# Optimization experiments

Measured on AMD Instinct MI355X. Metric: run time of the kernel, lower is better.

## Reference

```python
import jax, jax.numpy as jnp
import numpy as np

N_QUBITS = 8
N_LAYERS = 3
N_CLASSES = 3
BATCH = 16384


def setup_inputs() -> dict:
    key = jax.random.key(0)
    k1, k2, k3, k4 = jax.random.split(key, 4)
    x = jax.random.uniform(k1, (BATCH, N_QUBITS), dtype=jnp.float32)  # PCA feats in [0,1]
    q_weights = jax.random.normal(k2, (N_LAYERS * 2 * N_QUBITS,), dtype=jnp.float32) * 0.1
    W = jax.random.normal(k3, (N_CLASSES, N_CLASSES), dtype=jnp.float32) / np.sqrt(N_CLASSES)
    b = jax.random.normal(k4, (N_CLASSES,), dtype=jnp.float32) * 0.1
    return {"x": x, "q_weights": q_weights, "W": W, "b": b}


def _ry(state, wire, theta):
    """Batched RY(theta) on `wire`. state: (B,)+(2,)*n, theta: (B,)."""
    ax = 1 + wire
    s0 = jnp.take(state, 0, axis=ax)
    s1 = jnp.take(state, 1, axis=ax)
    bshape = (theta.shape[0],) + (1,) * (s0.ndim - 1)
    c = jnp.cos(0.5 * theta).reshape(bshape)
    s = jnp.sin(0.5 * theta).reshape(bshape)
    return jnp.stack([c * s0 - s * s1, s * s0 + c * s1], axis=ax)


def _rz(state, wire, theta):
    """RZ(theta) on `wire`, theta scalar: diag(e^{-i t/2}, e^{i t/2})."""
    ax = 1 + wire
    phases = jnp.stack([jnp.exp(-0.5j * theta), jnp.exp(0.5j * theta)])
    shape = (1,) * ax + (2,) + (1,) * (state.ndim - ax - 1)
    return state * phases.reshape(shape)


def _cnot(state, ctrl, tgt):
    """CNOT: flip target bit on the control=1 slice."""
    cax = 1 + ctrl
    a0 = jnp.take(state, 0, axis=cax)
    a1 = jnp.take(state, 1, axis=cax)
    # control axis was removed; target axis shifts down by one if tgt > ctrl
    tax = 1 + tgt if tgt < ctrl else tgt
    a1 = jnp.flip(a1, axis=tax)
    return jnp.stack([a0, a1], axis=cax)


def _circuit(x, q_weights):
    B = x.shape[0]
    state = jnp.zeros((B, 2 ** N_QUBITS), dtype=jnp.complex64).at[:, 0].set(1.0)
    state = state.reshape((B,) + (2,) * N_QUBITS)
    for layer in range(N_LAYERS):
        base = layer * 2 * N_QUBITS
        for i in range(N_QUBITS):
            state = _ry(state, i, x[:, i] * np.pi + q_weights[base + i])
        for i in range(N_QUBITS - 1):
            state = _cnot(state, i, i + 1)
        state = _cnot(state, N_QUBITS - 1, 0)
        for i in range(N_QUBITS):
            state = _rz(state, i, q_weights[base + N_QUBITS + i])
    probs = state.real ** 2 + state.imag ** 2  # (B,)+(2,)*n
    zs = []
    for i in range(N_CLASSES):
        ax = 1 + i
        p = probs.sum(axis=tuple(a for a in range(1, N_QUBITS + 1) if a != ax))  # (B,2)
        zs.append(p[:, 0] - p[:, 1])  # <Z_i>
    return jnp.stack(zs, axis=1).astype(jnp.float32)  # (B, n_classes)


def reference(x, q_weights, W, b):
    q_out = _circuit(x, q_weights)
    return q_out @ W.T + b
```

## Files before the change

### kernel.cpp

```cpp
#include <hip/hip_runtime.h>
#include <math.h>

#define NQ 8
#define NL 3
#define NC 3
#define BATCH 16384


__device__ __forceinline__ int par(int x) { return __popc(x) & 1; }

template<int CTRL>
__device__ __forceinline__ float dppmov(float v) {
  return __builtin_bit_cast(float,
    __builtin_amdgcn_update_dpp(0, __builtin_bit_cast(int, v), CTRL, 0xF, 0xF, true));
}

template<int M>
__device__ __forceinline__ float xl(float v) {
  static_assert(M > 0 && M < 64, "mask range");
  if constexpr (M < 16) {
    constexpr int hi = M & 12;
    constexpr int first = (hi == 0) ? 0 : (hi == 4) ? 0x141
                          : (hi == 8) ? 0x128
                          : 0x140;
    constexpr int qx = (hi == 4 || hi == 12) ? ((M & 3) ^ 3) : (M & 3);
    constexpr int qc = (qx == 1) ? 0xB1 : (qx == 2) ? 0x4E : 0x1B;
    float t = v;
    if constexpr (first != 0) t = dppmov<first>(t);
    if constexpr (qx != 0)    t = dppmov<qc>(t);
    return t;
  } else if constexpr (M < 32) {
    return __builtin_bit_cast(float,
      __builtin_amdgcn_ds_swizzle(__builtin_bit_cast(int, v), (M << 10) | 0x1F));
  } else {
    const int li = (int)(threadIdx.x & 63);
    return __builtin_bit_cast(float,
      __builtin_amdgcn_ds_bpermute(((li ^ M) << 2), __builtin_bit_cast(int, v)));
  }
}


template<int UREG, int GREG, int GLANE>
__device__ __forceinline__ void ry_rr(float (&sr)[4], float (&si)[4],
                                      float c, float s, int q) {
  static_assert((__builtin_popcount(UREG & GREG) & 1) == 1, "<g,u>!=1");
  const float sl = par(q & GLANE) ? s : -s;
  #pragma unroll
  for (int rA = 0; rA < 4; ++rA) {
    if (rA < (rA ^ UREG)) {
      const int rB = rA ^ UREG;
      const float FA = (__builtin_popcount(rA & GREG) & 1) ? -sl : sl;
      const float ar = sr[rA], ai = si[rA];
      sr[rA] = c * ar + FA * sr[rB];
      si[rA] = c * ai + FA * si[rB];
      sr[rB] = c * sr[rB] - FA * ar;
      si[rB] = c * si[rB] - FA * ai;
    }
  }
}

template<int ULANE, int GREG, int GLANE>
__device__ __forceinline__ void ry_ll(float (&sr)[4], float (&si)[4],
                                      float c, float s, int q) {
  static_assert((__builtin_popcount(ULANE & GLANE) & 1) == 1, "<g,u>!=1");
  const float sl = par(q & GLANE) ? s : -s;
  #pragma unroll
  for (int r = 0; r < 4; ++r) {
    const float xr = xl<ULANE>(sr[r]);
    const float xi = xl<ULANE>(si[r]);
    const float F  = (__builtin_popcount(r & GREG) & 1) ? -sl : sl;
    sr[r] = c * sr[r] + F * xr;
    si[r] = c * si[r] + F * xi;
  }
}

template<int UREG, int ULANE, int GREG, int GLANE>
__device__ __forceinline__ void ry_mix(float (&sr)[4], float (&si)[4],
                                       float c, float s, int q) {
  static_assert(((__builtin_popcount(UREG & GREG) + __builtin_popcount(ULANE & GLANE)) & 1) == 1,
                "<g,u>!=1");
  constexpr int RFLIP = __builtin_popcount(GREG & UREG) & 1;
  const float sl = par(q & GLANE) ? s : -s;
  #pragma unroll
  for (int rA = 0; rA < 4; ++rA) {
    if (rA < (rA ^ UREG)) {
      const int rB = rA ^ UREG;
      const float pBr = xl<ULANE>(sr[rB]);
      const float pBi = xl<ULANE>(si[rB]);
      const float pAr = xl<ULANE>(sr[rA]);
      const float pAi = xl<ULANE>(si[rA]);
      const float FA = (__builtin_popcount(rA & GREG) & 1) ? -sl : sl;
      const float FB = RFLIP ? -FA : FA;
      sr[rA] = c * sr[rA] + FA * pBr;
      si[rA] = c * si[rA] + FA * pBi;
      sr[rB] = c * sr[rB] + FB * pAr;
      si[rB] = c * si[rB] + FB * pAi;
    }
  }
}

__global__ __launch_bounds__(256, 6) void vqc_kernel(
    const float* __restrict__ x, const float* __restrict__ qw,
    const float* __restrict__ W, const float* __restrict__ b,
    float* __restrict__ out)
{
  const int tid  = threadIdx.x;
  const int q    = tid & 63;
  const int elem = blockIdx.x * 4 + (tid >> 6);

  const float PI = 3.14159265358979323846f;

  float xs[8];
  {
    const float4 x0 = *(const float4*)(x + elem * 8);
    const float4 x1 = *(const float4*)(x + elem * 8 + 4);
    xs[0] = x0.x; xs[1] = x0.y; xs[2] = x0.z; xs[3] = x0.w;
    xs[4] = x1.x; xs[5] = x1.y; xs[6] = x1.z; xs[7] = x1.w;
  }

  float sr[4], si[4];

  {
    float c0_, s0_, c1_, s1_;
    __sincosf(0.5f * (PI * xs[0] + qw[0]), &s0_, &c0_);
    __sincosf(0.5f * (PI * xs[1] + qw[1]), &s1_, &c1_);
    float P = 1.f;
    #pragma unroll
    for (int w = 2; w < 8; ++w) {
      float s_, c_;
      __sincosf(0.5f * (PI * xs[w] + qw[w]), &s_, &c_);
      P *= ((q >> (w - 2)) & 1) ? s_ : c_;
    }
    sr[0] = P * c0_ * c1_;
    sr[1] = P * s0_ * c1_;
    sr[2] = P * c0_ * s1_;
    sr[3] = P * s0_ * s1_;
  }

  {
    const float h0 = 0.5f * qw[8],  h1 = 0.5f * qw[9];
    const float h2 = 0.5f * qw[10], h3 = 0.5f * qw[11];
    const float h4 = 0.5f * qw[12], h5 = 0.5f * qw[13];
    const float h6 = 0.5f * qw[14], h7 = 0.5f * qw[15];
    const float a0 = par(q & 63) ? h0 : -h0;
    const float B  = -h1 + (par(q & 1)  ? h2 : -h2) + (par(q & 3)  ? h3 : -h3)
                         + (par(q & 7)  ? h4 : -h4) + (par(q & 15) ? h5 : -h5)
                         + (par(q & 31) ? h6 : -h6) + (par(q & 63) ? h7 : -h7);
    float sp0, cp0, sp1, cp1;
    __sincosf(a0 + B, &sp0, &cp0);
    __sincosf(a0 - B, &sp1, &cp1);
    si[0] =  sp0 * sr[0]; sr[0] *= cp0;
    si[1] =  sp1 * sr[1]; sr[1] *= cp1;
    si[2] = -sp0 * sr[2]; sr[2] *= cp0;
    si[3] = -sp1 * sr[3]; sr[3] *= cp1;
  }

  {
    float c_, s_;
    __sincosf(0.5f * (PI * xs[0] + qw[16]), &s_, &c_); ry_rr <3,     2, 63>(sr, si, c_, s_, q);
    __sincosf(0.5f * (PI * xs[1] + qw[17]), &s_, &c_); ry_mix<2, 1,  3,  0>(sr, si, c_, s_, q);
    __sincosf(0.5f * (PI * xs[2] + qw[18]), &s_, &c_); ry_ll <3,     3,  1>(sr, si, c_, s_, q);
    __sincosf(0.5f * (PI * xs[3] + qw[19]), &s_, &c_); ry_ll <6,     3,  3>(sr, si, c_, s_, q);
    __sincosf(0.5f * (PI * xs[4] + qw[20]), &s_, &c_); ry_ll <12,    3,  7>(sr, si, c_, s_, q);
    __sincosf(0.5f * (PI * xs[5] + qw[21]), &s_, &c_); ry_ll <24,    3, 15>(sr, si, c_, s_, q);
    __sincosf(0.5f * (PI * xs[6] + qw[22]), &s_, &c_); ry_ll <48,    3, 31>(sr, si, c_, s_, q);
    __sincosf(0.5f * (PI * xs[7] + qw[23]), &s_, &c_); ry_mix<3, 32, 3, 63>(sr, si, c_, s_, q);
  }

  {
    const float h0 = 0.5f * qw[24], h1 = 0.5f * qw[25];
    const float h2 = 0.5f * qw[26], h3 = 0.5f * qw[27];
    const float h4 = 0.5f * qw[28], h5 = 0.5f * qw[29];
    const float h6 = 0.5f * qw[30], h7 = 0.5f * qw[31];
    const float t0 = par(q & 42) ? h0 : -h0;
    const float D1 = (par(q & 63) ? h1 : -h1) + (par(q & 61) ? h3 : -h3)
                   + (par(q & 53) ? h5 : -h5) + (par(q & 21) ? h7 : -h7);
    const float D2 = (par(q & 62) ? h2 : -h2) + (par(q & 58) ? h4 : -h4)
                   + (par(q & 42) ? h6 : -h6);
    const float ph[4] = { t0 + D1 + D2, -t0 - D1 + D2,
                          -t0 + D1 - D2,  t0 - D1 - D2 };
    #pragma unroll
    for (int r = 0; r < 4; ++r) {
      float sp, cp;
      __sincosf(ph[r], &sp, &cp);
      const float re = sr[r], im = si[r];
      sr[r] = cp * re - sp * im;
      si[r] = cp * im + sp * re;
    }
  }

  {
    float c_, s_;
    __sincosf(0.5f * (PI * xs[0] + qw[32]), &s_, &c_); ry_mix<1, 1,  3, 42>(sr, si, c_, s_, q);
    __sincosf(0.5f * (PI * xs[1] + qw[33]), &s_, &c_); ry_mix<2, 2,  1, 63>(sr, si, c_, s_, q);
    __sincosf(0.5f * (PI * xs[2] + qw[34]), &s_, &c_); ry_ll <5,     2, 62>(sr, si, c_, s_, q);
    __sincosf(0.5f * (PI * xs[3] + qw[35]), &s_, &c_); ry_ll <10,    1, 61>(sr, si, c_, s_, q);
    __sincosf(0.5f * (PI * xs[4] + qw[36]), &s_, &c_); ry_ll <20,    2, 58>(sr, si, c_, s_, q);
    __sincosf(0.5f * (PI * xs[5] + qw[37]), &s_, &c_); ry_ll <40,    1, 53>(sr, si, c_, s_, q);
    __sincosf(0.5f * (PI * xs[6] + qw[38]), &s_, &c_); ry_mix<3, 16, 2, 42>(sr, si, c_, s_, q);
    __sincosf(0.5f * (PI * xs[7] + qw[39]), &s_, &c_); ry_mix<2, 33, 1, 21>(sr, si, c_, s_, q);
  }

  const float p0 = sr[0] * sr[0] + si[0] * si[0];
  const float p1 = sr[1] * sr[1] + si[1] * si[1];
  const float p2 = sr[2] * sr[2] + si[2] * si[2];
  const float p3 = sr[3] * sr[3] + si[3] * si[3];
  const float ta = (p0 + p1) - (p2 + p3);
  const float tb =  p0 + p1 + p2 + p3;
  float z0 = par(q & 12) ? -ta : ta;
  float z1 = par(q & 21) ? -ta : ta;
  float z2 = par(q & 43) ? -tb : tb;

  z0 += xl<1>(z0);  z1 += xl<1>(z1);  z2 += xl<1>(z2);
  z0 += xl<2>(z0);  z1 += xl<2>(z1);  z2 += xl<2>(z2);
  z0 += xl<4>(z0);  z1 += xl<4>(z1);  z2 += xl<4>(z2);
  z0 += xl<8>(z0);  z1 += xl<8>(z1);  z2 += xl<8>(z2);
  z0 += xl<16>(z0); z1 += xl<16>(z1); z2 += xl<16>(z2);
  z0 += xl<32>(z0); z1 += xl<32>(z1); z2 += xl<32>(z2);

  if (q < NC) {
    out[elem * NC + q] = b[q] + W[q * 3 + 0] * z0 + W[q * 3 + 1] * z1
                              + W[q * 3 + 2] * z2;
  }
}

extern "C" void kernel_launch(void* const* d_in, const int* in_sizes, int n_in,
                              void* d_out, int out_size, void* d_ws, size_t ws_size,
                              hipStream_t stream) {
  const float* x  = (const float*)d_in[0];
  const float* qw = (const float*)d_in[1];
  const float* W  = (const float*)d_in[2];
  const float* b  = (const float*)d_in[3];
  float* out = (float*)d_out;

  dim3 grid(BATCH / 4);
  vqc_kernel<<<grid, 256, 0, stream>>>(x, qw, W, b, out);
}
```

Measured before the change: 26.48 us.

## Use permlane swaps for cross-row exchanges, batch sincos, raise occupancy bound

Replaces ds_swizzle/ds_bpermute lane exchanges for masks 16 and 32 with permlane16/32 swap builtins when available. Exchanges whose mask mixes high and low bits become a chain of permlane and DPP moves. The per-gate sincos calls are hoisted into batched arrays ahead of each RY layer so transcendental latency can overlap, and launch bounds move from 6 to 8 waves. The aim is to avoid LDS-path shuffle latency and raise ILP and occupancy, at the cost of more live registers and possible spills under the tighter bound.

```diff
diff --git a/kernel.cpp b/kernel.cpp
--- a/kernel.cpp
+++ b/kernel.cpp
@@ -15,28 +15,51 @@
     __builtin_amdgcn_update_dpp(0, __builtin_bit_cast(int, v), CTRL, 0xF, 0xF, true));
 }
 
+__device__ __forceinline__ float pl16(float v) {
+#if __has_builtin(__builtin_amdgcn_permlane16_swap)
+  typedef int i2 __attribute__((ext_vector_type(2)));
+  const int iv = __builtin_bit_cast(int, v);
+  i2 pr = __builtin_amdgcn_permlane16_swap(iv, iv, false, false);
+  const int lane = (int)(threadIdx.x & 63);
+  return __builtin_bit_cast(float, (lane & 16) ? pr[0] : pr[1]);
+#else
+  return __builtin_bit_cast(float,
+    __builtin_amdgcn_ds_swizzle(__builtin_bit_cast(int, v), (16 << 10) | 0x1F));
+#endif
+}
+
+__device__ __forceinline__ float pl32(float v) {
+#if __has_builtin(__builtin_amdgcn_permlane32_swap)
+  typedef int i2 __attribute__((ext_vector_type(2)));
+  const int iv = __builtin_bit_cast(int, v);
+  i2 pr = __builtin_amdgcn_permlane32_swap(iv, iv, false, false);
+  const int lane = (int)(threadIdx.x & 63);
+  return __builtin_bit_cast(float, (lane & 32) ? pr[0] : pr[1]);
+#else
+  const int li = (int)(threadIdx.x & 63);
+  return __builtin_bit_cast(float,
+    __builtin_amdgcn_ds_bpermute(((li ^ 32) << 2), __builtin_bit_cast(int, v)));
+#endif
+}
+
 template<int M>
 __device__ __forceinline__ float xl(float v) {
   static_assert(M > 0 && M < 64, "mask range");
-  if constexpr (M < 16) {
-    constexpr int hi = M & 12;
+  float t = v;
+  if constexpr ((M & 32) != 0) t = pl32(t);
+  if constexpr ((M & 16) != 0) t = pl16(t);
+  if constexpr ((M & 15) != 0) {
+    constexpr int Ml = M & 15;
+    constexpr int hi = Ml & 12;
     constexpr int first = (hi == 0) ? 0 : (hi == 4) ? 0x141
                           : (hi == 8) ? 0x128
                           : 0x140;
-    constexpr int qx = (hi == 4 || hi == 12) ? ((M & 3) ^ 3) : (M & 3);
+    constexpr int qx = (hi == 4 || hi == 12) ? ((Ml & 3) ^ 3) : (Ml & 3);
     constexpr int qc = (qx == 1) ? 0xB1 : (qx == 2) ? 0x4E : 0x1B;
-    float t = v;
     if constexpr (first != 0) t = dppmov<first>(t);
     if constexpr (qx != 0)    t = dppmov<qc>(t);
-    return t;
-  } else if constexpr (M < 32) {
-    return __builtin_bit_cast(float,
-      __builtin_amdgcn_ds_swizzle(__builtin_bit_cast(int, v), (M << 10) | 0x1F));
-  } else {
-    const int li = (int)(threadIdx.x & 63);
-    return __builtin_bit_cast(float,
-      __builtin_amdgcn_ds_bpermute(((li ^ M) << 2), __builtin_bit_cast(int, v)));
-  }
+  }
+  return t;
 }
 
 
@@ -99,7 +122,7 @@
   }
 }
 
-__global__ __launch_bounds__(256, 6) void vqc_kernel(
+__global__ __launch_bounds__(256, 8) void vqc_kernel(
     const float* __restrict__ x, const float* __restrict__ qw,
     const float* __restrict__ W, const float* __restrict__ b,
     float* __restrict__ out)
@@ -121,20 +144,20 @@
   float sr[4], si[4];
 
   {
-    float c0_, s0_, c1_, s1_;
-    __sincosf(0.5f * (PI * xs[0] + qw[0]), &s0_, &c0_);
-    __sincosf(0.5f * (PI * xs[1] + qw[1]), &s1_, &c1_);
-    float P = 1.f;
-    #pragma unroll
-    for (int w = 2; w < 8; ++w) {
-      float s_, c_;
-      __sincosf(0.5f * (PI * xs[w] + qw[w]), &s_, &c_);
-      P *= ((q >> (w - 2)) & 1) ? s_ : c_;
-    }
-    sr[0] = P * c0_ * c1_;
-    sr[1] = P * s0_ * c1_;
-    sr[2] = P * c0_ * s1_;
-    sr[3] = P * s0_ * s1_;
+    float cw[8], sw[8];
+    #pragma unroll
+    for (int w = 0; w < 8; ++w)
+      __sincosf(0.5f * (PI * xs[w] + qw[w]), &sw[w], &cw[w]);
+    float P = ((q & 1)  ? sw[2] : cw[2]);
+    P      *= ((q & 2)  ? sw[3] : cw[3]);
+    P      *= ((q & 4)  ? sw[4] : cw[4]);
+    P      *= ((q & 8)  ? sw[5] : cw[5]);
+    P      *= ((q & 16) ? sw[6] : cw[6]);
+    P      *= ((q & 32) ? sw[7] : cw[7]);
+    sr[0] = P * cw[0] * cw[1];
+    sr[1] = P * sw[0] * cw[1];
+    sr[2] = P * cw[0] * sw[1];
+    sr[3] = P * sw[0] * sw[1];
   }
 
   {
@@ -156,15 +179,19 @@
   }
 
   {
-    float c_, s_;
-    __sincosf(0.5f * (PI * xs[0] + qw[16]), &s_, &c_); ry_rr <3,     2, 63>(sr, si, c_, s_, q);
-    __sincosf(0.5f * (PI * xs[1] + qw[17]), &s_, &c_); ry_mix<2, 1,  3,  0>(sr, si, c_, s_, q);
-    __sincosf(0.5f * (PI * xs[2] + qw[18]), &s_, &c_); ry_ll <3,     3,  1>(sr, si, c_, s_, q);
-    __sincosf(0.5f * (PI * xs[3] + qw[19]), &s_, &c_); ry_ll <6,     3,  3>(sr, si, c_, s_, q);
-    __sincosf(0.5f * (PI * xs[4] + qw[20]), &s_, &c_); ry_ll <12,    3,  7>(sr, si, c_, s_, q);
-    __sincosf(0.5f * (PI * xs[5] + qw[21]), &s_, &c_); ry_ll <24,    3, 15>(sr, si, c_, s_, q);
-    __sincosf(0.5f * (PI * xs[6] + qw[22]), &s_, &c_); ry_ll <48,    3, 31>(sr, si, c_, s_, q);
-    __sincosf(0.5f * (PI * xs[7] + qw[23]), &s_, &c_); ry_mix<3, 32, 3, 63>(sr, si, c_, s_, q);
+    float cw[8], sw[8];
+    #pragma unroll
+    for (int w = 0; w < 8; ++w)
+      __sincosf(0.5f * (PI * xs[w] + qw[16 + w]), &sw[w], &cw[w]);
+
+    ry_rr <3,     2, 63>(sr, si, cw[0], sw[0], q);
+    ry_mix<2, 1,  3,  0>(sr, si, cw[1], sw[1], q);
+    ry_ll <3,     3,  1>(sr, si, cw[2], sw[2], q);
+    ry_ll <6,     3,  3>(sr, si, cw[3], sw[3], q);
+    ry_ll <12,    3,  7>(sr, si, cw[4], sw[4], q);
+    ry_ll <24,    3, 15>(sr, si, cw[5], sw[5], q);
+    ry_ll <48,    3, 31>(sr, si, cw[6], sw[6], q);
+    ry_mix<3, 32, 3, 63>(sr, si, cw[7], sw[7], q);
   }
 
   {
@@ -190,15 +217,19 @@
   }
 
   {
-    float c_, s_;
-    __sincosf(0.5f * (PI * xs[0] + qw[32]), &s_, &c_); ry_mix<1, 1,  3, 42>(sr, si, c_, s_, q);
-    __sincosf(0.5f * (PI * xs[1] + qw[33]), &s_, &c_); ry_mix<2, 2,  1, 63>(sr, si, c_, s_, q);
-    __sincosf(0.5f * (PI * xs[2] + qw[34]), &s_, &c_); ry_ll <5,     2, 62>(sr, si, c_, s_, q);
-    __sincosf(0.5f * (PI * xs[3] + qw[35]), &s_, &c_); ry_ll <10,    1, 61>(sr, si, c_, s_, q);
-    __sincosf(0.5f * (PI * xs[4] + qw[36]), &s_, &c_); ry_ll <20,    2, 58>(sr, si, c_, s_, q);
-    __sincosf(0.5f * (PI * xs[5] + qw[37]), &s_, &c_); ry_ll <40,    1, 53>(sr, si, c_, s_, q);
-    __sincosf(0.5f * (PI * xs[6] + qw[38]), &s_, &c_); ry_mix<3, 16, 2, 42>(sr, si, c_, s_, q);
-    __sincosf(0.5f * (PI * xs[7] + qw[39]), &s_, &c_); ry_mix<2, 33, 1, 21>(sr, si, c_, s_, q);
+    float cw[8], sw[8];
+    #pragma unroll
+    for (int w = 0; w < 8; ++w)
+      __sincosf(0.5f * (PI * xs[w] + qw[32 + w]), &sw[w], &cw[w]);
+
+    ry_mix<1, 1,  3, 42>(sr, si, cw[0], sw[0], q);
+    ry_mix<2, 2,  1, 63>(sr, si, cw[1], sw[1], q);
+    ry_ll <5,     2, 62>(sr, si, cw[2], sw[2], q);
+    ry_ll <10,    1, 61>(sr, si, cw[3], sw[3], q);
+    ry_ll <20,    2, 58>(sr, si, cw[4], sw[4], q);
+    ry_ll <40,    1, 53>(sr, si, cw[5], sw[5], q);
+    ry_mix<3, 16, 2, 42>(sr, si, cw[6], sw[6], q);
+    ry_mix<2, 33, 1, 21>(sr, si, cw[7], sw[7], q);
   }
 
   const float p0 = sr[0] * sr[0] + si[0] * si[0];
```

Result: slower. 35.60 us (+34.4%).
